# Kernel optimization log

Measured on AMD Instinct MI355X. Metric: run time of the kernel, lower is better.

Reference implementation:

```python
import jax, jax.numpy as jnp
import numpy as np

B, N, D = 4, 4096, 1024
LN_EPS = 1e-5

def setup_inputs() -> dict:
    key = jax.random.key(0)
    ks = jax.random.split(key, 12)
    s = 1.0 / np.sqrt(D)
    return {
        "embeddings": jax.random.normal(ks[0], (B, N, D), dtype=jnp.float32),
        "edge_indices": jax.random.randint(ks[1], (2, 8192), 0, N, dtype=jnp.int64),
        "edge_times": jax.random.uniform(ks[2], (8192,), dtype=jnp.float32),
        "timestamps": jax.random.uniform(ks[3], (N,), dtype=jnp.float32),
        "Wq": jax.random.uniform(ks[4], (D, D), jnp.float32, -s, s),
        "bq": jax.random.uniform(ks[5], (D,), jnp.float32, -s, s),
        "Wk": jax.random.uniform(ks[6], (D, D), jnp.float32, -s, s),
        "bk": jax.random.uniform(ks[7], (D,), jnp.float32, -s, s),
        "Wv": jax.random.uniform(ks[8], (D, D), jnp.float32, -s, s),
        "bv": jax.random.uniform(ks[9], (D,), jnp.float32, -s, s),
        "gamma": jnp.ones((D,), jnp.float32),
        "beta": jnp.zeros((D,), jnp.float32),
    }

def reference(embeddings, edge_indices, edge_times, timestamps,
              Wq, bq, Wk, bk, Wv, bv, gamma, beta):
    # edge_indices / edge_times / timestamps are unused by the original forward.
    d = embeddings.shape[-1]
    q = jnp.einsum("bnd,ed->bne", embeddings, Wq) + bq   # [B,N,D]
    k = jnp.einsum("bnd,ed->bne", embeddings, Wk) + bk
    v = jnp.einsum("bnd,ed->bne", embeddings, Wv) + bv
    scores = jnp.einsum("bnd,bmd->bnm", q, k) / jnp.sqrt(jnp.asarray(d, embeddings.dtype))
    attn = jax.nn.softmax(scores, axis=-1)                # [B,N,N]
    attended = jnp.einsum("bnm,bmd->bnd", attn, v)
    x = embeddings + attended
    mu = jnp.mean(x, axis=-1, keepdims=True)
    var = jnp.mean(jnp.square(x - mu), axis=-1, keepdims=True)
    return gamma * (x - mu) * jax.lax.rsqrt(var + LN_EPS) + beta
```

## Files before the change

kernel.cpp:

```cpp
#include <hip/hip_runtime.h>
#include <hip/hip_fp8.h>

typedef unsigned short u16;
typedef unsigned char  u8;
typedef long long      i64;
using bf16x8 = __attribute__((ext_vector_type(8))) __bf16;
using f32x4  = __attribute__((ext_vector_type(4))) float;

__device__ __forceinline__ u16 f2bf(float f) {
    unsigned u = __builtin_bit_cast(unsigned, f);
    u += 0x7fffu + ((u >> 16) & 1u);
    return (u16)(u >> 16);
}
__device__ __forceinline__ float bf2f(u16 h) {
    unsigned u = ((unsigned)h) << 16;
    return __builtin_bit_cast(float, u);
}
__device__ __forceinline__ u8 f2fp8(float f) {
    __hip_fp8_e4m3 t(f);
    return t.__x;
}
__device__ __forceinline__ float wred_sum(float v) {
    #pragma unroll
    for (int o = 32; o; o >>= 1) v += __shfl_xor(v, o, 64);
    return v;
}

__device__ __forceinline__ void gl2lds16(const void* g, void* l) {
    __builtin_amdgcn_global_load_lds(
        (__attribute__((address_space(1))) void*)(g),
        (__attribute__((address_space(3))) void*)(l), 16, 0, 0);
}

__global__ __launch_bounds__(256)
void cast_bf16(const float* __restrict__ src, u16* __restrict__ dst, int n4) {
    int i = blockIdx.x * 256 + threadIdx.x;
    if (i < n4) {
        float4 f = ((const float4*)src)[i];
        ushort4 u;
        u.x = f2bf(f.x); u.y = f2bf(f.y); u.z = f2bf(f.z); u.w = f2bf(f.w);
        ((ushort4*)dst)[i] = u;
    }
}

__global__ __launch_bounds__(256)
void cast_v_fp8(const u16* __restrict__ src, u8* __restrict__ dst, int n8) {
    int i = blockIdx.x * 256 + threadIdx.x;
    if (i < n8) {
        ushort4 a = ((const ushort4*)src)[2 * i];
        ushort4 b = ((const ushort4*)src)[2 * i + 1];
        union { u8 c[8]; unsigned long long q; } r;
        r.c[0] = f2fp8(bf2f(a.x)); r.c[1] = f2fp8(bf2f(a.y));
        r.c[2] = f2fp8(bf2f(a.z)); r.c[3] = f2fp8(bf2f(a.w));
        r.c[4] = f2fp8(bf2f(b.x)); r.c[5] = f2fp8(bf2f(b.y));
        r.c[6] = f2fp8(bf2f(b.z)); r.c[7] = f2fp8(bf2f(b.w));
        ((unsigned long long*)dst)[i] = r.q;
    }
}

template<int MODE, int TM, bool SWAP>
__global__ __launch_bounds__(256, 4)
void gemm_bt(const u16* __restrict__ A, const u16* __restrict__ Bt, const int K,
             u16* __restrict__ oQ, u16* __restrict__ oK, u16* __restrict__ oVt,
             const float* __restrict__ bQ, const float* __restrict__ bK,
             const float* __restrict__ bV,
             u8* __restrict__ oP, float* __restrict__ sums, const float scale)
{
    __shared__ u16 smem[TM * 32 + 128 * 32];
    u16* As = smem;
    u16* Bs = smem + TM * 32;

    constexpr int IM = TM / 32;
    const int tid  = threadIdx.x;
    const int wv   = tid >> 6;
    const int lane = tid & 63;
    const int wr   = (wv >> 1) * (TM / 2);
    const int wc   = (wv & 1) << 6;

    const int row0 = (SWAP ? blockIdx.x : blockIdx.y) * TM;
    const int col0 = (SWAP ? blockIdx.y : blockIdx.x) * 128;

    const int srow = tid >> 2;
    const int scol = (((tid & 3) ^ ((tid >> 3) & 3)) << 3);

    const u16* pA0 = A  + (size_t)(row0 + srow) * K + scol;
    const u16* pB0 = Bt + (size_t)(col0 + srow) * K + scol;

    char* aB0 = (char*)As + wv * 1024;
    char* aB1 = (char*)As + 4096 + wv * 1024;
    char* bB0 = (char*)Bs + wv * 1024;
    char* bB1 = (char*)Bs + 4096 + wv * 1024;

    const int fr = lane & 15;
    const int g  = lane >> 4;
    const int sw = (fr >> 1) & 3;
    const int kc = ((g ^ sw) << 3);

    f32x4 acc[IM][4];
    #pragma unroll
    for (int i = 0; i < IM; i++)
        #pragma unroll
        for (int j = 0; j < 4; j++) acc[i][j] = (f32x4){0.f, 0.f, 0.f, 0.f};

    for (int k0 = 0; k0 < K; k0 += 32) {
        __syncthreads();
        gl2lds16(pA0 + k0, aB0);
        if (TM == 128) gl2lds16(pA0 + (size_t)64 * K + k0, aB1);
        gl2lds16(pB0 + k0, bB0);
        gl2lds16(pB0 + (size_t)64 * K + k0, bB1);
        __syncthreads();

        bf16x8 af[IM], bfr[4];
        #pragma unroll
        for (int i = 0; i < IM; i++) af[i]  = *(const bf16x8*)&As[(wr + 16 * i + fr) * 32 + kc];
        #pragma unroll
        for (int j = 0; j < 4; j++)  bfr[j] = *(const bf16x8*)&Bs[(wc + 16 * j + fr) * 32 + kc];
        #pragma unroll
        for (int i = 0; i < IM; i++)
            #pragma unroll
            for (int j = 0; j < 4; j++)
                acc[i][j] = __builtin_amdgcn_mfma_f32_16x16x32_bf16(af[i], bfr[j], acc[i][j], 0, 0, 0);
    }

    const int rB = (lane >> 4) << 2;
    const int cB = lane & 15;

    if (MODE == 0) {
        const int sel = col0 >> 10;
        if (sel < 2) {
            const float* bias = (sel == 0) ? bQ : bK;
            u16* dst = (sel == 0) ? oQ : oK;
            #pragma unroll
            for (int i = 0; i < IM; i++) {
                #pragma unroll
                for (int j = 0; j < 4; j++) {
                    const int m0 = row0 + wr + 16 * i + rB;
                    const int e  = (col0 & 1023) + wc + 16 * j + cB;
                    const float bb = bias[e];
                    #pragma unroll
                    for (int t = 0; t < 4; t++)
                        dst[(size_t)(m0 + t) * 1024 + e] = f2bf(acc[i][j][t] + bb);
                }
            }
        } else {
            const int b      = row0 >> 12;
            const int n_base = row0 & 4095;
            const int e0     = col0 & 1023;
            __syncthreads();
            #pragma unroll
            for (int P = 0; P < 2; ++P) {
                if ((wc >> 6) == P) {
                    #pragma unroll
                    for (int i = 0; i < IM; i++) {
                        const int n_l0 = wr + 16 * i + rB;
                        const int hq   = n_l0 >> 3;
                        const int off  = n_l0 & 7;
                        #pragma unroll
                        for (int j = 0; j < 4; j++) {
                            const int e_p = 16 * j + cB;
                            const int hp  = hq ^ (e_p & 7);
                            const float bb = bV[e0 + P * 64 + e_p];
                            ushort4 pk;
                            pk.x = f2bf(acc[i][j][0] + bb);
                            pk.y = f2bf(acc[i][j][1] + bb);
                            pk.z = f2bf(acc[i][j][2] + bb);
                            pk.w = f2bf(acc[i][j][3] + bb);
                            *(ushort4*)&smem[e_p * 128 + hp * 8 + off] = pk;
                        }
                    }
                }
                __syncthreads();
                #pragma unroll
                for (int p4 = 0; p4 < 4; ++p4) {
                    const int idx = p4 * 256 + tid;
                    const int er  = idx >> 4;
                    const int c   = idx & 15;
                    const int cc  = c ^ (er & 7);
                    int4 v = *(const int4*)&smem[er * 128 + cc * 8];
                    *(int4*)&oVt[(size_t)b * 4194304 +
                                 (size_t)(e0 + P * 64 + er) * 4096 + n_base + c * 8] = v;
                }
                if (P == 0) __syncthreads();
            }
        }
    }
}

__global__ __launch_bounds__(512, 2)
void gemm_s8(const u16* __restrict__ Q, const u16* __restrict__ Km,
             u8* __restrict__ P, float* __restrict__ sm, const float scale)
{
    __shared__ u16 smem[65536];
    const int tid = threadIdx.x;
    const int wv = tid >> 6, lane = tid & 63;
    const int wm = wv >> 2, wn = wv & 3;
    const int row0 = blockIdx.x << 8, col0 = blockIdx.y << 8;

    const int srow = tid >> 2;
    const int scol = ((tid & 3) ^ ((tid >> 3) & 3)) << 3;
    const u16* gA = Q  + (size_t)(row0 + srow) * 1024 + scol;
    const u16* gB = Km + (size_t)(col0 + srow) * 1024 + scol;
    char* lds = (char*)smem;
    const int wvo = wv << 10;

    const int fr = lane & 15, g = lane >> 4;
    const int kc = (g ^ ((fr >> 1) & 3)) << 4;

    f32x4 acc[8][4];
    #pragma unroll
    for (int i = 0; i < 8; i++)
        #pragma unroll
        for (int j = 0; j < 4; j++) acc[i][j] = (f32x4){0.f, 0.f, 0.f, 0.f};

    #define SG_A(ts, sl) { \
        gl2lds16(gA + (ts) * 32,          lds + (sl) * 32768 + wvo); \
        gl2lds16(gA + 131072 + (ts) * 32, lds + (sl) * 32768 + 8192 + wvo); }
    #define SG_B(ts, sl) { \
        gl2lds16(gB + (ts) * 32,          lds + (sl) * 32768 + 16384 + wvo); \
        gl2lds16(gB + 131072 + (ts) * 32, lds + (sl) * 32768 + 24576 + wvo); }

    SG_A(0, 0); SG_B(0, 0);
    SG_A(1, 1); SG_B(1, 1);
    SG_A(2, 2); SG_B(2, 2);

    for (int t = 0; t < 32; ++t) {
        const int slot = t & 3;
        const int ts = (t + 3) & 31;
        const int ns = (t + 3) & 3;
        const char* Ab = lds + slot * 32768;
        const char* Bb = Ab + 16384;

        asm volatile("s_waitcnt vmcnt(8)" ::: "memory");
        __builtin_amdgcn_s_barrier();
        __builtin_amdgcn_sched_barrier(0);

        SG_A(ts, ns);
        bf16x8 bf[4], af[4];
        #pragma unroll
        for (int j = 0; j < 4; ++j)
            bf[j] = *(const bf16x8*)(Bb + (wn * 64 + 16 * j + fr) * 64 + kc);
        #pragma unroll
        for (int i = 0; i < 4; ++i)
            af[i] = *(const bf16x8*)(Ab + (wm * 128 + 16 * i + fr) * 64 + kc);
        __builtin_amdgcn_s_setprio(1);
        #pragma unroll
        for (int i = 0; i < 4; ++i)
            #pragma unroll
            for (int j = 0; j < 4; ++j)
                acc[i][j] = __builtin_amdgcn_mfma_f32_16x16x32_bf16(af[i], bf[j], acc[i][j], 0, 0, 0);
        __builtin_amdgcn_s_setprio(0);
        __builtin_amdgcn_s_barrier();

        SG_B(ts, ns);
        #pragma unroll
        for (int i = 0; i < 4; ++i)
            af[i] = *(const bf16x8*)(Ab + (wm * 128 + 64 + 16 * i + fr) * 64 + kc);
        __builtin_amdgcn_s_setprio(1);
        #pragma unroll
        for (int i = 0; i < 4; ++i)
            #pragma unroll
            for (int j = 0; j < 4; ++j)
                acc[i + 4][j] = __builtin_amdgcn_mfma_f32_16x16x32_bf16(af[i], bf[j], acc[i + 4][j], 0, 0, 0);
        __builtin_amdgcn_s_setprio(0);
    }
    #undef SG_A
    #undef SG_B

    const int rB = (lane >> 4) << 2, cB = lane & 15;
    float psum[8][4];
    #pragma unroll
    for (int i = 0; i < 8; i++)
        #pragma unroll
        for (int t = 0; t < 4; t++) psum[i][t] = 0.f;

    #pragma unroll
    for (int i = 0; i < 8; i++) {
        const int m0 = row0 + wm * 128 + 16 * i + rB;
        #pragma unroll
        for (int j = 0; j < 4; j++) {
            const int c = col0 + wn * 64 + 16 * j + cB;
            #pragma unroll
            for (int t = 0; t < 4; t++) {
                const float e = __expf(acc[i][j][t] * scale);
                psum[i][t] += e;
                P[(size_t)(m0 + t) * 4096 + c] = f2fp8(e);
            }
        }
    }
    #pragma unroll
    for (int i = 0; i < 8; i++) {
        #pragma unroll
        for (int t = 0; t < 4; t++) {
            float v = psum[i][t];
            v += __shfl_xor(v, 1, 64);
            v += __shfl_xor(v, 2, 64);
            v += __shfl_xor(v, 4, 64);
            v += __shfl_xor(v, 8, 64);
            if (cB == 0)
                atomicAdd(&sm[row0 + wm * 128 + 16 * i + rB + t], v);
        }
    }
}

__global__ __launch_bounds__(512, 2)
void pv8(const u8* __restrict__ p0, const u8* __restrict__ p1,
         const u8* __restrict__ p2, const u8* __restrict__ p3,
         const u8* __restrict__ vt8, const float* __restrict__ sums,
         float* __restrict__ out)
{
    __shared__ u8 smem[131072];
    const int b = blockIdx.z;
    const u8* Pb = (b == 0) ? p0 : (b == 1) ? p1 : (b == 2) ? p2 : p3;
    const u8* Vb = vt8 + (size_t)b * 4194304;
    const float* sm = sums + (b << 12);
    float* Ob = out + (size_t)b * 4194304;

    const int tid = threadIdx.x;
    const int wv = tid >> 6, lane = tid & 63;
    const int wm = wv >> 2, wn = wv & 3;
    const int row0 = blockIdx.x << 8, col0 = blockIdx.y << 8;

    const int srow = tid >> 2;
    const int sc16 = ((tid & 3) ^ ((tid >> 3) & 3)) << 4;
    const u8* gA = Pb + (size_t)(row0 + srow) * 4096 + sc16;
    const u8* gB = Vb + (size_t)(col0 + srow) * 4096 + sc16;
    char* lds = (char*)smem;
    const int wvo = wv << 10;

    const int fr = lane & 15, g = lane >> 4;
    const int sw = (fr >> 1) & 3;
    const int g2 = g >> 1, h8 = (g & 1) << 3;
    const int pc0 = ((g2 ^ sw) << 4) + h8;
    const int pc1 = (((2 + g2) ^ sw) << 4) + h8;

    f32x4 acc[8][4];
    #pragma unroll
    for (int i = 0; i < 8; i++)
        #pragma unroll
        for (int j = 0; j < 4; j++) acc[i][j] = (f32x4){0.f, 0.f, 0.f, 0.f};

    #define PG_A(ts, sl) { \
        gl2lds16(gA + (ts) * 64,          lds + (sl) * 32768 + wvo); \
        gl2lds16(gA + 524288 + (ts) * 64, lds + (sl) * 32768 + 8192 + wvo); }
    #define PG_B(ts, sl) { \
        gl2lds16(gB + (ts) * 64,          lds + (sl) * 32768 + 16384 + wvo); \
        gl2lds16(gB + 524288 + (ts) * 64, lds + (sl) * 32768 + 24576 + wvo); }

    PG_A(0, 0); PG_B(0, 0);
    PG_A(1, 1); PG_B(1, 1);
    PG_A(2, 2); PG_B(2, 2);

    for (int t = 0; t < 64; ++t) {
        const int slot = t & 3;
        const int ts = (t + 3) & 63;
        const int ns = (t + 3) & 3;
        const char* Ab = lds + slot * 32768;
        const char* Bb = Ab + 16384;

        asm volatile("s_waitcnt vmcnt(8)" ::: "memory");
        __builtin_amdgcn_s_barrier();
        __builtin_amdgcn_sched_barrier(0);

        PG_A(ts, ns);
        i64 af[8], bf[4];
        #pragma unroll
        for (int i = 0; i < 8; ++i) af[i] = *(const i64*)(Ab + (wm * 128 + 16 * i + fr) * 64 + pc0);
        #pragma unroll
        for (int j = 0; j < 4; ++j) bf[j] = *(const i64*)(Bb + (wn * 64 + 16 * j + fr) * 64 + pc0);
        __builtin_amdgcn_s_setprio(1);
        #pragma unroll
        for (int i = 0; i < 8; ++i)
            #pragma unroll
            for (int j = 0; j < 4; ++j)
                acc[i][j] = __builtin_amdgcn_mfma_f32_16x16x32_fp8_fp8(af[i], bf[j], acc[i][j], 0, 0, 0);
        __builtin_amdgcn_s_setprio(0);
        __builtin_amdgcn_s_barrier();

        PG_B(ts, ns);
        #pragma unroll
        for (int i = 0; i < 8; ++i) af[i] = *(const i64*)(Ab + (wm * 128 + 16 * i + fr) * 64 + pc1);
        #pragma unroll
        for (int j = 0; j < 4; ++j) bf[j] = *(const i64*)(Bb + (wn * 64 + 16 * j + fr) * 64 + pc1);
        __builtin_amdgcn_s_setprio(1);
        #pragma unroll
        for (int i = 0; i < 8; ++i)
            #pragma unroll
            for (int j = 0; j < 4; ++j)
                acc[i][j] = __builtin_amdgcn_mfma_f32_16x16x32_fp8_fp8(af[i], bf[j], acc[i][j], 0, 0, 0);
        __builtin_amdgcn_s_setprio(0);
    }
    #undef PG_A
    #undef PG_B

    const int rB = (lane >> 4) << 2, cB = lane & 15;
    #pragma unroll
    for (int i = 0; i < 8; i++) {
        const int m0 = row0 + wm * 128 + 16 * i + rB;
        const float i0 = 1.0f / sm[m0];
        const float i1 = 1.0f / sm[m0 + 1];
        const float i2 = 1.0f / sm[m0 + 2];
        const float i3 = 1.0f / sm[m0 + 3];
        #pragma unroll
        for (int j = 0; j < 4; j++) {
            const int e = col0 + wn * 64 + 16 * j + cB;
            Ob[(size_t)(m0 + 0) * 1024 + e] = acc[i][j][0] * i0;
            Ob[(size_t)(m0 + 1) * 1024 + e] = acc[i][j][1] * i1;
            Ob[(size_t)(m0 + 2) * 1024 + e] = acc[i][j][2] * i2;
            Ob[(size_t)(m0 + 3) * 1024 + e] = acc[i][j][3] * i3;
        }
    }
}

__global__ __launch_bounds__(256)
void residual_ln(const float* __restrict__ emb, float* __restrict__ out,
                 const float* __restrict__ gamma, const float* __restrict__ beta) {
    const size_t row = blockIdx.x;
    const int t = threadIdx.x;
    const int wv = t >> 6, lane = t & 63;
    const size_t base = row * 1024 + t * 4;

    float4 ev = *(const float4*)(emb + base);
    float4 ov = *(const float4*)(out + base);
    float x0 = ev.x + ov.x, x1 = ev.y + ov.y, x2 = ev.z + ov.z, x3 = ev.w + ov.w;

    float s = x0 + x1 + x2 + x3;
    float q = x0 * x0 + x1 * x1 + x2 * x2 + x3 * x3;
    s = wred_sum(s);
    q = wred_sum(q);
    __shared__ float s1[4], s2[4];
    if (lane == 0) { s1[wv] = s; s2[wv] = q; }
    __syncthreads();
    s = s1[0] + s1[1] + s1[2] + s1[3];
    q = s2[0] + s2[1] + s2[2] + s2[3];

    const float mu  = s * (1.0f / 1024.0f);
    const float var = q * (1.0f / 1024.0f) - mu * mu;
    const float r   = rsqrtf(var + 1e-5f);

    float4 g  = *(const float4*)(gamma + t * 4);
    float4 be = *(const float4*)(beta + t * 4);
    float4 res;
    res.x = (x0 - mu) * r * g.x + be.x;
    res.y = (x1 - mu) * r * g.y + be.y;
    res.z = (x2 - mu) * r * g.z + be.z;
    res.w = (x3 - mu) * r * g.w + be.w;
    *(float4*)(out + base) = res;
}

extern "C" void kernel_launch(void* const* d_in, const int* in_sizes, int n_in,
                              void* d_out, int out_size, void* d_ws, size_t ws_size,
                              hipStream_t stream) {
    const float* emb   = (const float*)d_in[0];
    const float* Wq    = (const float*)d_in[4];
    const float* bq    = (const float*)d_in[5];
    const float* Wk    = (const float*)d_in[6];
    const float* bk    = (const float*)d_in[7];
    const float* Wv    = (const float*)d_in[8];
    const float* bv    = (const float*)d_in[9];
    const float* gamma = (const float*)d_in[10];
    const float* beta  = (const float*)d_in[11];
    float* out = (float*)d_out;

    char* ws = (char*)d_ws;
    if (ws_size < 140509184u) return;
    u16* Xbf = (u16*)(ws);
    u16* Wbf = (u16*)(ws + 33554432);
    u16* Qbf = (u16*)(ws + 39845888);
    u16* Kbf = (u16*)(ws + 73400320);
    u16* VTB = (u16*)(ws + 106954752);

    u8*    VT8  = (u8*)(ws);
    u8*    P0   = (u8*)(ws + 16777216);
    float* SUMS = (float*)(ws + 33554432);
    u8*    P1   = (u8*)(ws + 106954752);
    u8*    P2   = (u8*)(ws + 123731968);
    u8*    P3   = (u8*)(ws + 39845888);
    u8*    Pb[4] = {P0, P1, P2, P3};

    cast_bf16<<<16384, 256, 0, stream>>>(emb, Xbf, 4194304);
    cast_bf16<<<1024, 256, 0, stream>>>(Wq, Wbf,           262144);
    cast_bf16<<<1024, 256, 0, stream>>>(Wk, Wbf + 1048576, 262144);
    cast_bf16<<<1024, 256, 0, stream>>>(Wv, Wbf + 2097152, 262144);

    gemm_bt<0, 128, true><<<dim3(128, 24), 256, 0, stream>>>(Xbf, Wbf, 1024,
        Qbf, Kbf, VTB, bq, bk, bv, nullptr, nullptr, 1.0f);

    cast_v_fp8<<<8192, 256, 0, stream>>>(VTB, VT8, 2097152);

    hipMemsetAsync(SUMS, 0, 65536, stream);

    for (int b = 0; b < 4; ++b) {
        const size_t o = (size_t)b * 4194304;
        gemm_s8<<<dim3(16, 16), 512, 0, stream>>>(Qbf + o, Kbf + o,
            Pb[b], SUMS + b * 4096, 0.03125f);
    }

    pv8<<<dim3(16, 4, 4), 512, 0, stream>>>(P0, P1, P2, P3, VT8, SUMS, out);

    residual_ln<<<16384, 256, 0, stream>>>(emb, out, gamma, beta);
}
```

Measured before the change: 602.0 us.

## Unify QKV projection with 256x256 pipelined GEMM and move barriers after LDS reads

Measured after the change: 589.5 us. 2.1% less time.

```diff
diff --git a/kernel.cpp b/kernel.cpp
--- a/kernel.cpp
+++ b/kernel.cpp
@@ -58,72 +58,100 @@
     }
 }
 
-template<int MODE, int TM, bool SWAP>
-__global__ __launch_bounds__(256, 4)
-void gemm_bt(const u16* __restrict__ A, const u16* __restrict__ Bt, const int K,
+template<int MODE>
+__global__ __launch_bounds__(512, 2)
+void gemm256(const u16* __restrict__ A, const u16* __restrict__ Bt,
              u16* __restrict__ oQ, u16* __restrict__ oK, u16* __restrict__ oVt,
              const float* __restrict__ bQ, const float* __restrict__ bK,
              const float* __restrict__ bV,
              u8* __restrict__ oP, float* __restrict__ sums, const float scale)
 {
-    __shared__ u16 smem[TM * 32 + 128 * 32];
-    u16* As = smem;
-    u16* Bs = smem + TM * 32;
-
-    constexpr int IM = TM / 32;
-    const int tid  = threadIdx.x;
-    const int wv   = tid >> 6;
-    const int lane = tid & 63;
-    const int wr   = (wv >> 1) * (TM / 2);
-    const int wc   = (wv & 1) << 6;
-
-    const int row0 = (SWAP ? blockIdx.x : blockIdx.y) * TM;
-    const int col0 = (SWAP ? blockIdx.y : blockIdx.x) * 128;
+    __shared__ u16 smem[65536];
+    const int tid = threadIdx.x;
+    const int wv = tid >> 6, lane = tid & 63;
+    const int wm = wv >> 2, wn = wv & 3;
+    const int row0 = blockIdx.x << 8, col0 = blockIdx.y << 8;
 
     const int srow = tid >> 2;
-    const int scol = (((tid & 3) ^ ((tid >> 3) & 3)) << 3);
-
-    const u16* pA0 = A  + (size_t)(row0 + srow) * K + scol;
-    const u16* pB0 = Bt + (size_t)(col0 + srow) * K + scol;
-
-    char* aB0 = (char*)As + wv * 1024;
-    char* aB1 = (char*)As + 4096 + wv * 1024;
-    char* bB0 = (char*)Bs + wv * 1024;
-    char* bB1 = (char*)Bs + 4096 + wv * 1024;
-
-    const int fr = lane & 15;
-    const int g  = lane >> 4;
-    const int sw = (fr >> 1) & 3;
-    const int kc = ((g ^ sw) << 3);
-
-    f32x4 acc[IM][4];
+    const int scol = ((tid & 3) ^ ((tid >> 3) & 3)) << 3;
+    const u16* gA = A  + (size_t)(row0 + srow) * 1024 + scol;
+    const u16* gB = Bt + (size_t)(col0 + srow) * 1024 + scol;
+    char* lds = (char*)smem;
+    const int wvo = wv << 10;
+
+    const int fr = lane & 15, g = lane >> 4;
+    const int kc = (g ^ ((fr >> 1) & 3)) << 4;
+
+    f32x4 acc[8][4];
     #pragma unroll
-    for (int i = 0; i < IM; i++)
+    for (int i = 0; i < 8; i++)
         #pragma unroll
         for (int j = 0; j < 4; j++) acc[i][j] = (f32x4){0.f, 0.f, 0.f, 0.f};
 
-    for (int k0 = 0; k0 < K; k0 += 32) {
-        __syncthreads();
-        gl2lds16(pA0 + k0, aB0);
-        if (TM == 128) gl2lds16(pA0 + (size_t)64 * K + k0, aB1);
-        gl2lds16(pB0 + k0, bB0);
-        gl2lds16(pB0 + (size_t)64 * K + k0, bB1);
-        __syncthreads();
-
-        bf16x8 af[IM], bfr[4];
-        #pragma unroll
-        for (int i = 0; i < IM; i++) af[i]  = *(const bf16x8*)&As[(wr + 16 * i + fr) * 32 + kc];
-        #pragma unroll
-        for (int j = 0; j < 4; j++)  bfr[j] = *(const bf16x8*)&Bs[(wc + 16 * j + fr) * 32 + kc];
-        #pragma unroll
-        for (int i = 0; i < IM; i++)
-            #pragma unroll
-            for (int j = 0; j < 4; j++)
-                acc[i][j] = __builtin_amdgcn_mfma_f32_16x16x32_bf16(af[i], bfr[j], acc[i][j], 0, 0, 0);
-    }
-
-    const int rB = (lane >> 4) << 2;
-    const int cB = lane & 15;
+    #define SG_A(ts, sl) { \
+        gl2lds16(gA + (ts) * 32,          lds + (sl) * 32768 + wvo); \
+        gl2lds16(gA + 131072 + (ts) * 32, lds + (sl) * 32768 + 8192 + wvo); }
+    #define SG_B(ts, sl) { \
+        gl2lds16(gB + (ts) * 32,          lds + (sl) * 32768 + 16384 + wvo); \
+        gl2lds16(gB + 131072 + (ts) * 32, lds + (sl) * 32768 + 24576 + wvo); }
+
+    SG_A(0, 0); SG_B(0, 0);
+    SG_A(1, 1); SG_B(1, 1);
+    SG_A(2, 2); SG_B(2, 2);
+    asm volatile("s_waitcnt vmcnt(8)" ::: "memory");
+    __builtin_amdgcn_s_barrier();
+
+    for (int t = 0; t < 32; ++t) {
+        const int slot = t & 3;
+        const int ts = (t + 3) & 31;
+        const int ns = (t + 3) & 3;
+        const char* Ab = lds + slot * 32768;
+        const char* Bb = Ab + 16384;
+
+        SG_A(ts, ns);
+        bf16x8 bf[4], af[4];
+        #pragma unroll
+        for (int j = 0; j < 4; ++j)
+            bf[j] = *(const bf16x8*)(Bb + (wn * 64 + 16 * j + fr) * 64 + kc);
+        #pragma unroll
+        for (int i = 0; i < 4; ++i)
+            af[i] = *(const bf16x8*)(Ab + (wm * 128 + 16 * i + fr) * 64 + kc);
+        __builtin_amdgcn_sched_barrier(0);
+        __builtin_amdgcn_s_barrier();
+        asm volatile("s_waitcnt lgkmcnt(0)" ::: "memory");
+        __builtin_amdgcn_sched_barrier(0);
+        __builtin_amdgcn_s_setprio(1);
+        #pragma unroll
+        for (int i = 0; i < 4; ++i)
+            #pragma unroll
+            for (int j = 0; j < 4; ++j)
+                acc[i][j] = __builtin_amdgcn_mfma_f32_16x16x32_bf16(af[i], bf[j], acc[i][j], 0, 0, 0);
+        __builtin_amdgcn_s_setprio(0);
+
+        SG_B(ts, ns);
+        bf16x8 af2[4];
+        #pragma unroll
+        for (int i = 0; i < 4; ++i)
+            af2[i] = *(const bf16x8*)(Ab + (wm * 128 + 64 + 16 * i + fr) * 64 + kc);
+        asm volatile("s_waitcnt vmcnt(8)" ::: "memory");
+        __builtin_amdgcn_sched_barrier(0);
+        __builtin_amdgcn_s_barrier();
+        asm volatile("s_waitcnt lgkmcnt(0)" ::: "memory");
+        __builtin_amdgcn_sched_barrier(0);
+        __builtin_amdgcn_s_setprio(1);
+        #pragma unroll
+        for (int i = 0; i < 4; ++i)
+            #pragma unroll
+            for (int j = 0; j < 4; ++j)
+                acc[i + 4][j] = __builtin_amdgcn_mfma_f32_16x16x32_bf16(af2[i], bf[j], acc[i + 4][j], 0, 0, 0);
+        __builtin_amdgcn_s_setprio(0);
+    }
+    #undef SG_A
+    #undef SG_B
+
+    asm volatile("s_waitcnt vmcnt(0)" ::: "memory");
+
+    const int rB = (lane >> 4) << 2, cB = lane & 15;
 
     if (MODE == 0) {
         const int sel = col0 >> 10;
@@ -131,11 +159,11 @@
             const float* bias = (sel == 0) ? bQ : bK;
             u16* dst = (sel == 0) ? oQ : oK;
             #pragma unroll
-            for (int i = 0; i < IM; i++) {
+            for (int i = 0; i < 8; i++) {
                 #pragma unroll
                 for (int j = 0; j < 4; j++) {
-                    const int m0 = row0 + wr + 16 * i + rB;
-                    const int e  = (col0 & 1023) + wc + 16 * j + cB;
+                    const int m0 = row0 + wm * 128 + 16 * i + rB;
+                    const int e  = (col0 & 1023) + wn * 64 + 16 * j + cB;
                     const float bb = bias[e];
                     #pragma unroll
                     for (int t = 0; t < 4; t++)
@@ -148,165 +176,77 @@
             const int e0     = col0 & 1023;
             __syncthreads();
             #pragma unroll
-            for (int P = 0; P < 2; ++P) {
-                if ((wc >> 6) == P) {
-                    #pragma unroll
-                    for (int i = 0; i < IM; i++) {
-                        const int n_l0 = wr + 16 * i + rB;
-                        const int hq   = n_l0 >> 3;
-                        const int off  = n_l0 & 7;
-                        #pragma unroll
-                        for (int j = 0; j < 4; j++) {
-                            const int e_p = 16 * j + cB;
-                            const int hp  = hq ^ (e_p & 7);
-                            const float bb = bV[e0 + P * 64 + e_p];
-                            ushort4 pk;
-                            pk.x = f2bf(acc[i][j][0] + bb);
-                            pk.y = f2bf(acc[i][j][1] + bb);
-                            pk.z = f2bf(acc[i][j][2] + bb);
-                            pk.w = f2bf(acc[i][j][3] + bb);
-                            *(ushort4*)&smem[e_p * 128 + hp * 8 + off] = pk;
-                        }
-                    }
+            for (int i = 0; i < 8; i++) {
+                const int n_l0 = wm * 128 + 16 * i + rB;
+                const int hq   = n_l0 >> 3;
+                const int off  = n_l0 & 7;
+                #pragma unroll
+                for (int j = 0; j < 4; j++) {
+                    const int e_p = wn * 64 + 16 * j + cB;
+                    const int hp  = hq ^ (e_p & 7);
+                    const float bb = bV[e0 + e_p];
+                    ushort4 pk;
+                    pk.x = f2bf(acc[i][j][0] + bb);
+                    pk.y = f2bf(acc[i][j][1] + bb);
+                    pk.z = f2bf(acc[i][j][2] + bb);
+                    pk.w = f2bf(acc[i][j][3] + bb);
+                    *(ushort4*)&smem[e_p * 256 + hp * 8 + off] = pk;
                 }
-                __syncthreads();
-                #pragma unroll
-                for (int p4 = 0; p4 < 4; ++p4) {
-                    const int idx = p4 * 256 + tid;
-                    const int er  = idx >> 4;
-                    const int c   = idx & 15;
-                    const int cc  = c ^ (er & 7);
-                    int4 v = *(const int4*)&smem[er * 128 + cc * 8];
-                    *(int4*)&oVt[(size_t)b * 4194304 +
-                                 (size_t)(e0 + P * 64 + er) * 4096 + n_base + c * 8] = v;
-                }
-                if (P == 0) __syncthreads();
+            }
+            __syncthreads();
+            #pragma unroll
+            for (int it = 0; it < 16; ++it) {
+                const int idx = it * 512 + tid;
+                const int er  = idx >> 5;
+                const int c   = idx & 31;
+                const int cc  = c ^ (er & 7);
+                int4 v = *(const int4*)&smem[er * 256 + cc * 8];
+                *(int4*)&oVt[(size_t)b * 4194304 +
+                             (size_t)(e0 + er) * 4096 + n_base + c * 8] = v;
             }
         }
-    }
-}
-
-__global__ __launch_bounds__(512, 2)
-void gemm_s8(const u16* __restrict__ Q, const u16* __restrict__ Km,
-             u8* __restrict__ P, float* __restrict__ sm, const float scale)
-{
-    __shared__ u16 smem[65536];
-    const int tid = threadIdx.x;
-    const int wv = tid >> 6, lane = tid & 63;
-    const int wm = wv >> 2, wn = wv & 3;
-    const int row0 = blockIdx.x << 8, col0 = blockIdx.y << 8;
-
-    const int srow = tid >> 2;
-    const int scol = ((tid & 3) ^ ((tid >> 3) & 3)) << 3;
-    const u16* gA = Q  + (size_t)(row0 + srow) * 1024 + scol;
-    const u16* gB = Km + (size_t)(col0 + srow) * 1024 + scol;
-    char* lds = (char*)smem;
-    const int wvo = wv << 10;
-
-    const int fr = lane & 15, g = lane >> 4;
-    const int kc = (g ^ ((fr >> 1) & 3)) << 4;
-
-    f32x4 acc[8][4];
-    #pragma unroll
-    for (int i = 0; i < 8; i++)
-        #pragma unroll
-        for (int j = 0; j < 4; j++) acc[i][j] = (f32x4){0.f, 0.f, 0.f, 0.f};
-
-    #define SG_A(ts, sl) { \
-        gl2lds16(gA + (ts) * 32,          lds + (sl) * 32768 + wvo); \
-        gl2lds16(gA + 131072 + (ts) * 32, lds + (sl) * 32768 + 8192 + wvo); }
-    #define SG_B(ts, sl) { \
-        gl2lds16(gB + (ts) * 32,          lds + (sl) * 32768 + 16384 + wvo); \
-        gl2lds16(gB + 131072 + (ts) * 32, lds + (sl) * 32768 + 24576 + wvo); }
-
-    SG_A(0, 0); SG_B(0, 0);
-    SG_A(1, 1); SG_B(1, 1);
-    SG_A(2, 2); SG_B(2, 2);
-
-    for (int t = 0; t < 32; ++t) {
-        const int slot = t & 3;
-        const int ts = (t + 3) & 31;
-        const int ns = (t + 3) & 3;
-        const char* Ab = lds + slot * 32768;
-        const char* Bb = Ab + 16384;
-
-        asm volatile("s_waitcnt vmcnt(8)" ::: "memory");
-        __builtin_amdgcn_s_barrier();
-        __builtin_amdgcn_sched_barrier(0);
-
-        SG_A(ts, ns);
-        bf16x8 bf[4], af[4];
-        #pragma unroll
-        for (int j = 0; j < 4; ++j)
-            bf[j] = *(const bf16x8*)(Bb + (wn * 64 + 16 * j + fr) * 64 + kc);
-        #pragma unroll
-        for (int i = 0; i < 4; ++i)
-            af[i] = *(const bf16x8*)(Ab + (wm * 128 + 16 * i + fr) * 64 + kc);
-        __builtin_amdgcn_s_setprio(1);
-        #pragma unroll
-        for (int i = 0; i < 4; ++i)
-            #pragma unroll
-            for (int j = 0; j < 4; ++j)
-                acc[i][j] = __builtin_amdgcn_mfma_f32_16x16x32_bf16(af[i], bf[j], acc[i][j], 0, 0, 0);
-        __builtin_amdgcn_s_setprio(0);
-        __builtin_amdgcn_s_barrier();
-
-        SG_B(ts, ns);
-        #pragma unroll
-        for (int i = 0; i < 4; ++i)
-            af[i] = *(const bf16x8*)(Ab + (wm * 128 + 64 + 16 * i + fr) * 64 + kc);
-        __builtin_amdgcn_s_setprio(1);
-        #pragma unroll
-        for (int i = 0; i < 4; ++i)
-            #pragma unroll
-            for (int j = 0; j < 4; ++j)
-                acc[i + 4][j] = __builtin_amdgcn_mfma_f32_16x16x32_bf16(af[i], bf[j], acc[i + 4][j], 0, 0, 0);
-        __builtin_amdgcn_s_setprio(0);
-    }
-    #undef SG_A
-    #undef SG_B
-
-    const int rB = (lane >> 4) << 2, cB = lane & 15;
-    float psum[8][4];
-    #pragma unroll
-    for (int i = 0; i < 8; i++)
-        #pragma unroll
-        for (int t = 0; t < 4; t++) psum[i][t] = 0.f;
-
-    #pragma unroll
-    for (int i = 0; i < 8; i++) {
-        const int m0 = row0 + wm * 128 + 16 * i + rB;
-        #pragma unroll
-        for (int j = 0; j < 4; j++) {
-            const int c = col0 + wn * 64 + 16 * j + cB;
-            #pragma unroll
-            for (int t = 0; t < 4; t++) {
-                const float e = __expf(acc[i][j][t] * scale);
-                psum[i][t] += e;
-                P[(size_t)(m0 + t) * 4096 + c] = f2fp8(e);
+    } else {
+        float psum[8][4];
+        #pragma unroll
+        for (int i = 0; i < 8; i++)
+            #pragma unroll
+            for (int t = 0; t < 4; t++) psum[i][t] = 0.f;
+
+        #pragma unroll
+        for (int i = 0; i < 8; i++) {
+            const int m0 = row0 + wm * 128 + 16 * i + rB;
+            #pragma unroll
+            for (int j = 0; j < 4; j++) {
+                const int c = col0 + wn * 64 + 16 * j + cB;
+                #pragma unroll
+                for (int t = 0; t < 4; t++) {
+                    const float e = __expf(acc[i][j][t] * scale);
+                    psum[i][t] += e;
+                    oP[(size_t)(m0 + t) * 4096 + c] = f2fp8(e);
+                }
             }
         }
-    }
-    #pragma unroll
-    for (int i = 0; i < 8; i++) {
-        #pragma unroll
-        for (int t = 0; t < 4; t++) {
-            float v = psum[i][t];
-            v += __shfl_xor(v, 1, 64);
-            v += __shfl_xor(v, 2, 64);
-            v += __shfl_xor(v, 4, 64);
-            v += __shfl_xor(v, 8, 64);
-            if (cB == 0)
-                atomicAdd(&sm[row0 + wm * 128 + 16 * i + rB + t], v);
+        #pragma unroll
+        for (int i = 0; i < 8; i++) {
+            #pragma unroll
+            for (int t = 0; t < 4; t++) {
+                float v = psum[i][t];
+                v += __shfl_xor(v, 1, 64);
+                v += __shfl_xor(v, 2, 64);
+                v += __shfl_xor(v, 4, 64);
+                v += __shfl_xor(v, 8, 64);
+                if (cB == 0)
+                    atomicAdd(&sums[row0 + wm * 128 + 16 * i + rB + t], v);
+            }
         }
     }
 }
 
 __global__ __launch_bounds__(512, 2)
-void pv8(const u8* __restrict__ p0, const u8* __restrict__ p1,
-         const u8* __restrict__ p2, const u8* __restrict__ p3,
-         const u8* __restrict__ vt8, const float* __restrict__ sums,
-         float* __restrict__ out)
+void pv256(const u8* __restrict__ p0, const u8* __restrict__ p1,
+           const u8* __restrict__ p2, const u8* __restrict__ p3,
+           const u8* __restrict__ vt8, const float* __restrict__ sums,
+           float* __restrict__ out)
 {
     __shared__ u8 smem[131072];
     const int b = blockIdx.z;
@@ -349,6 +289,8 @@
     PG_A(0, 0); PG_B(0, 0);
     PG_A(1, 1); PG_B(1, 1);
     PG_A(2, 2); PG_B(2, 2);
+    asm volatile("s_waitcnt vmcnt(8)" ::: "memory");
+    __builtin_amdgcn_s_barrier();
 
     for (int t = 0; t < 64; ++t) {
         const int slot = t & 3;
@@ -357,16 +299,16 @@
         const char* Ab = lds + slot * 32768;
         const char* Bb = Ab + 16384;
 
-        asm volatile("s_waitcnt vmcnt(8)" ::: "memory");
-        __builtin_amdgcn_s_barrier();
-        __builtin_amdgcn_sched_barrier(0);
-
         PG_A(ts, ns);
         i64 af[8], bf[4];
         #pragma unroll
         for (int i = 0; i < 8; ++i) af[i] = *(const i64*)(Ab + (wm * 128 + 16 * i + fr) * 64 + pc0);
         #pragma unroll
         for (int j = 0; j < 4; ++j) bf[j] = *(const i64*)(Bb + (wn * 64 + 16 * j + fr) * 64 + pc0);
+        __builtin_amdgcn_sched_barrier(0);
+        __builtin_amdgcn_s_barrier();
+        asm volatile("s_waitcnt lgkmcnt(0)" ::: "memory");
+        __builtin_amdgcn_sched_barrier(0);
         __builtin_amdgcn_s_setprio(1);
         #pragma unroll
         for (int i = 0; i < 8; ++i)
@@ -374,13 +316,17 @@
             for (int j = 0; j < 4; ++j)
                 acc[i][j] = __builtin_amdgcn_mfma_f32_16x16x32_fp8_fp8(af[i], bf[j], acc[i][j], 0, 0, 0);
         __builtin_amdgcn_s_setprio(0);
+
+        PG_B(ts, ns);
+        #pragma unroll
+        for (int i = 0; i < 8; ++i) af[i] = *(const i64*)(Ab + (wm * 128 + 16 * i + fr) * 64 + pc1);
+        #pragma unroll
+        for (int j = 0; j < 4; ++j) bf[j] = *(const i64*)(Bb + (wn * 64 + 16 * j + fr) * 64 + pc1);
+        asm volatile("s_waitcnt vmcnt(8)" ::: "memory");
+        __builtin_amdgcn_sched_barrier(0);
         __builtin_amdgcn_s_barrier();
-
-        PG_B(ts, ns);
-        #pragma unroll
-        for (int i = 0; i < 8; ++i) af[i] = *(const i64*)(Ab + (wm * 128 + 16 * i + fr) * 64 + pc1);
-        #pragma unroll
-        for (int j = 0; j < 4; ++j) bf[j] = *(const i64*)(Bb + (wn * 64 + 16 * j + fr) * 64 + pc1);
+        asm volatile("s_waitcnt lgkmcnt(0)" ::: "memory");
+        __builtin_amdgcn_sched_barrier(0);
         __builtin_amdgcn_s_setprio(1);
         #pragma unroll
         for (int i = 0; i < 8; ++i)
@@ -391,6 +337,8 @@
     }
     #undef PG_A
     #undef PG_B
+
+    asm volatile("s_waitcnt vmcnt(0)" ::: "memory");
 
     const int rB = (lane >> 4) << 2, cB = lane & 15;
     #pragma unroll
@@ -482,7 +430,7 @@
     cast_bf16<<<1024, 256, 0, stream>>>(Wk, Wbf + 1048576, 262144);
     cast_bf16<<<1024, 256, 0, stream>>>(Wv, Wbf + 2097152, 262144);
 
-    gemm_bt<0, 128, true><<<dim3(128, 24), 256, 0, stream>>>(Xbf, Wbf, 1024,
+    gemm256<0><<<dim3(64, 12), 512, 0, stream>>>(Xbf, Wbf,
         Qbf, Kbf, VTB, bq, bk, bv, nullptr, nullptr, 1.0f);
 
     cast_v_fp8<<<8192, 256, 0, stream>>>(VTB, VT8, 2097152);
@@ -491,11 +439,12 @@
 
     for (int b = 0; b < 4; ++b) {
         const size_t o = (size_t)b * 4194304;
-        gemm_s8<<<dim3(16, 16), 512, 0, stream>>>(Qbf + o, Kbf + o,
+        gemm256<1><<<dim3(16, 16), 512, 0, stream>>>(Qbf + o, Kbf + o,
+            nullptr, nullptr, nullptr, nullptr, nullptr, nullptr,
             Pb[b], SUMS + b * 4096, 0.03125f);
     }
 
-    pv8<<<dim3(16, 4, 4), 512, 0, stream>>>(P0, P1, P2, P3, VT8, SUMS, out);
+    pv256<<<dim3(16, 4, 4), 512, 0, stream>>>(P0, P1, P2, P3, VT8, SUMS, out);
 
     residual_ln<<<16384, 256, 0, stream>>>(emb, out, gamma, beta);
 }
```
